# Kernel tuning notes

Measured on AMD Instinct MI355X. Metric: run time of the kernel, lower is better.

## Reference

```python
import jax, jax.numpy as jnp
import numpy as np

B, N, HID, E, H = 4, 256, 256, 64, 4
OUT = HID // 2          # 128
D = OUT // H            # 32
AGG = H * (2 * D + 1)   # 260 = concat(mean D, attn_sum 1, max D) per head


def setup_inputs() -> dict:
    key = jax.random.key(0)
    ks = jax.random.split(key, 7)
    s = 0.05
    return {
        "h_x": jax.random.normal(ks[0], (B, N, HID), jnp.float32),
        "h_e": jax.random.normal(ks[1], (B, N, N, E), jnp.float32),
        "h_m": jnp.ones((B, N), jnp.float32),
        "W_Q": jax.random.normal(ks[2], (OUT, HID), jnp.float32) * s,
        "W_K": jax.random.normal(ks[3], (OUT, E), jnp.float32) * s,
        "W_V": jax.random.normal(ks[4], (OUT, E), jnp.float32) * s,
        "W_R": jax.random.normal(ks[5], (OUT, AGG), jnp.float32) * s,
    }


def reference(h_x, h_e, h_m, W_Q, W_K, W_V, W_R):
    # queries from node features: [B,H,N,D]
    h_q = (h_x @ W_Q.T).reshape(B, N, H, D).transpose(0, 2, 1, 3)
    # keys/values from dense pairwise edge features: [B,H,N,N,D]
    h_k = jnp.einsum('bnme,ce->bnmc', h_e, W_K).reshape(B, N, N, H, D).transpose(0, 3, 1, 2, 4)
    h_v = jnp.einsum('bnme,ce->bnmc', h_e, W_V).reshape(B, N, N, H, D).transpose(0, 3, 1, 2, 4)
    # broadcast dot: [B,H,N,N]
    scores = jnp.einsum('bhnd,bhnmd->bhnm', h_q, h_k) / np.float32(np.sqrt(D))
    # per-node mask broadcast as [B,1,N,1] (masks query rows)
    scores = jnp.where(h_m[:, None, :, None] == 0, -jnp.inf, scores)
    # NOTE: original code softmaxes over dim=1 = HEAD axis (faithful)
    attn = jax.nn.softmax(scores, axis=1)                      # [B,H,N,N]
    attn_w = attn[..., None] * h_v                             # [B,H,N,N,D]
    aggr_sum = attn_w.sum(axis=3)                              # [B,H,N,D]
    attn_sum = attn.sum(axis=3, keepdims=True) + 1e-8          # [B,H,N,1]
    aggr_mean = aggr_sum / attn_sum
    aggr_max = attn_w.max(axis=3)                              # [B,H,N,D]
    multi = jnp.concatenate([aggr_mean, attn_sum, aggr_max], axis=-1)  # [B,H,N,2D+1]
    aggr_out = multi.transpose(0, 2, 1, 3).reshape(B, N, AGG)  # [B,N,260]
    return aggr_out @ W_R.T                                    # [B,N,OUT]
```

## Files before the change

kernel.cpp:

```cpp
#include <hip/hip_runtime.h>

constexpr int Bb   = 4;
constexpr int Nn   = 256;
constexpr int HID  = 256;
constexpr int Ee   = 64;
constexpr int Hh   = 4;
constexpr int OUTc = 128;
constexpr int Dd   = 32;
constexpr int AGG  = 260;

constexpr int MT    = 32;
constexpr int A_LD  = 72;
constexpr int KV_LD = 260;

typedef __attribute__((ext_vector_type(8))) short short8;
typedef __attribute__((ext_vector_type(4))) float floatx4;

__device__ __forceinline__ unsigned short f2bf(float f) {
    union { float f; unsigned u; } x; x.f = f;
    unsigned r = x.u + 0x7FFFu + ((x.u >> 16) & 1u);
    return (unsigned short)(r >> 16);
}

__device__ __forceinline__ short8 pack8(floatx4 f0, floatx4 f1) {
    short8 v;
    v[0] = (short)f2bf(f0[0]); v[1] = (short)f2bf(f0[1]);
    v[2] = (short)f2bf(f0[2]); v[3] = (short)f2bf(f0[3]);
    v[4] = (short)f2bf(f1[0]); v[5] = (short)f2bf(f1[1]);
    v[6] = (short)f2bf(f1[2]); v[7] = (short)f2bf(f1[3]);
    return v;
}

__global__ __launch_bounds__(256, 3)
void eama_fused(const float* __restrict__ h_x, const float* __restrict__ h_e,
                const float* __restrict__ h_m, const float* __restrict__ W_Q,
                const float* __restrict__ W_K, const float* __restrict__ W_V,
                const float* __restrict__ W_R, float* __restrict__ out)
{
    __shared__ __align__(16) unsigned short sA[MT * A_LD];
    __shared__ __align__(16) float sKV[MT * KV_LD];
    __shared__ __align__(16) float sQ[OUTc];
    __shared__ float sSc[MT][4];
    __shared__ float sAt[MT][4];
    __shared__ float sAsum[Hh];
    __shared__ float sRed[2][OUTc];
    __shared__ __align__(16) float sMulti[AGG];

    const int tid  = threadIdx.x;
    const int lane = tid & 63;
    const int wv   = tid >> 6;
    const int bn   = blockIdx.x;
    const float maskv = h_m[bn];

    short8 bfrag[4][2];
    {
        const int ncol = lane & 15;
        const int q8   = lane >> 4;
        #pragma unroll
        for (int ct = 0; ct < 4; ++ct) {
            const int c = wv * 64 + ct * 16 + ncol;
            const float* row = (c < OUTc) ? (W_K + c * Ee) : (W_V + (c - OUTc) * Ee);
            #pragma unroll
            for (int ks = 0; ks < 2; ++ks) {
                const int k0 = ks * 32 + q8 * 8;
                floatx4 f0 = *(const floatx4*)(row + k0);
                floatx4 f1 = *(const floatx4*)(row + k0 + 4);
                bfrag[ct][ks] = pack8(f0, f1);
            }
        }
    }

    {
        float* sHx = sKV;
        sHx[tid] = h_x[bn * HID + tid];
        __syncthreads();
        if (tid < OUTc) {
            const float* wq = W_Q + tid * HID;
            float acc = 0.f;
            #pragma unroll 8
            for (int e = 0; e < HID; e += 4) {
                floatx4 w4 = *(const floatx4*)(wq + e);
                floatx4 x4 = *(const floatx4*)(sHx + e);
                acc += w4[0]*x4[0] + w4[1]*x4[1] + w4[2]*x4[2] + w4[3]*x4[3];
            }
            sQ[tid] = acc;
        }
        __syncthreads();
    }

    float vsum = 0.f, vmax = -3.402823466e38f;
    float asum_acc = 0.f;
    const int hf = tid >> 7;
    const int cp = tid & 127;
    const int hd = cp >> 5;

    const float* heb = h_e + (size_t)bn * (Nn * Ee);

    for (int tile = 0; tile < Nn / MT; ++tile) {
        const int m0 = tile * MT;
        __syncthreads();
        {
            const int r = tid >> 3, blk = tid & 7;
            const float* src = heb + (m0 + r) * Ee + blk * 8;
            floatx4 f0 = *(const floatx4*)(src);
            floatx4 f1 = *(const floatx4*)(src + 4);
            *(short8*)&sA[r * A_LD + blk * 8] = pack8(f0, f1);
        }
        __syncthreads();
        {
            const int ncol = lane & 15;
            const int q8   = lane >> 4;
            floatx4 acc[2][4];
            #pragma unroll
            for (int mt = 0; mt < 2; ++mt)
                #pragma unroll
                for (int ct = 0; ct < 4; ++ct)
                    acc[mt][ct] = (floatx4){0.f, 0.f, 0.f, 0.f};
            #pragma unroll
            for (int ks = 0; ks < 2; ++ks) {
                short8 a0 = *(const short8*)&sA[(ncol) * A_LD + ks * 32 + q8 * 8];
                short8 a1 = *(const short8*)&sA[(16 + ncol) * A_LD + ks * 32 + q8 * 8];
                #pragma unroll
                for (int ct = 0; ct < 4; ++ct) {
                    acc[0][ct] = __builtin_amdgcn_mfma_f32_16x16x32_bf16(a0, bfrag[ct][ks], acc[0][ct], 0, 0, 0);
                    acc[1][ct] = __builtin_amdgcn_mfma_f32_16x16x32_bf16(a1, bfrag[ct][ks], acc[1][ct], 0, 0, 0);
                }
            }
            #pragma unroll
            for (int mt = 0; mt < 2; ++mt) {
                const int rowb = mt * 16 + q8 * 4;
                #pragma unroll
                for (int ct = 0; ct < 4; ++ct) {
                    const int col = wv * 64 + ct * 16 + ncol;
                    #pragma unroll
                    for (int r = 0; r < 4; ++r)
                        sKV[(rowb + r) * KV_LD + col] = acc[mt][ct][r];
                }
            }
        }
        __syncthreads();
        if (tid < 128) {
            const int m = tid & 31, h = tid >> 5;
            const float* kvr = &sKV[m * KV_LD + h * Dd];
            const float* qr  = &sQ[h * Dd];
            float p = 0.f;
            #pragma unroll
            for (int d = 0; d < Dd; d += 4) {
                floatx4 k4 = *(const floatx4*)(kvr + d);
                floatx4 q4 = *(const floatx4*)(qr + d);
                p += k4[0]*q4[0] + k4[1]*q4[1] + k4[2]*q4[2] + k4[3]*q4[3];
            }
            p *= 0.1767766952966369f;
            sSc[m][h] = (maskv != 0.f) ? p : -1e30f;
        }
        __syncthreads();
        if (tid < MT) {
            float s0 = sSc[tid][0], s1 = sSc[tid][1], s2 = sSc[tid][2], s3 = sSc[tid][3];
            float mx = fmaxf(fmaxf(s0, s1), fmaxf(s2, s3));
            float e0 = __expf(s0 - mx), e1 = __expf(s1 - mx);
            float e2 = __expf(s2 - mx), e3 = __expf(s3 - mx);
            float inv = 1.f / (e0 + e1 + e2 + e3);
            sAt[tid][0] = e0 * inv; sAt[tid][1] = e1 * inv;
            sAt[tid][2] = e2 * inv; sAt[tid][3] = e3 * inv;
        }
        __syncthreads();
        #pragma unroll
        for (int mm = 0; mm < MT / 2; ++mm) {
            const int m = hf * (MT / 2) + mm;
            const float a  = sAt[m][hd];
            const float vv = sKV[m * KV_LD + OUTc + cp];
            const float aw = a * vv;
            vsum += aw;
            vmax = fmaxf(vmax, aw);
        }
        if (tid < Hh) {
            #pragma unroll
            for (int m = 0; m < MT; ++m) asum_acc += sAt[m][tid];
        }
    }

    __syncthreads();
    if (hf) { sRed[0][cp] = vsum; sRed[1][cp] = vmax; }
    if (tid < Hh) sAsum[tid] = asum_acc + 1e-8f;
    __syncthreads();
    if (tid < OUTc) {
        const float vs = vsum + sRed[0][tid];
        const float vm = fmaxf(vmax, sRed[1][tid]);
        const int h = tid >> 5, d = tid & 31;
        sMulti[h * 65 + d]      = vs / sAsum[h];
        sMulti[h * 65 + 33 + d] = vm;
        if (tid < Hh) sMulti[tid * 65 + 32] = sAsum[tid];
    }
    __syncthreads();
    if (tid < OUTc) {
        const float* wr = W_R + tid * AGG;
        float acc = 0.f;
        #pragma unroll 5
        for (int j = 0; j < AGG; j += 4) {
            floatx4 w4 = *(const floatx4*)(wr + j);
            floatx4 m4 = *(const floatx4*)(&sMulti[j]);
            acc += w4[0]*m4[0] + w4[1]*m4[1] + w4[2]*m4[2] + w4[3]*m4[3];
        }
        out[bn * OUTc + tid] = acc;
    }
}

extern "C" void kernel_launch(void* const* d_in, const int* in_sizes, int n_in,
                              void* d_out, int out_size, void* d_ws, size_t ws_size,
                              hipStream_t stream) {
    const float* h_x = (const float*)d_in[0];
    const float* h_e = (const float*)d_in[1];
    const float* h_m = (const float*)d_in[2];
    const float* W_Q = (const float*)d_in[3];
    const float* W_K = (const float*)d_in[4];
    const float* W_V = (const float*)d_in[5];
    const float* W_R = (const float*)d_in[6];
    float* out = (float*)d_out;
    eama_fused<<<dim3(Bb * Nn), dim3(256), 0, stream>>>(h_x, h_e, h_m, W_Q, W_K, W_V, W_R, out);
}
```

Measured before the change: 151.0 us.

## Split fused kernel into Q projection, split-N partial stage, and reduction stage

Moves the Q projection into a separate batched kernel and splits the per-node loop over neighbor tiles across a second grid dimension, so each block handles only 64 neighbors and writes partial sum/max/attention-sum records to workspace. A third kernel reduces the partials and applies W_R. Inside stage1, the V half is consumed straight from MFMA accumulators with shuffle reductions instead of being staged through shared memory, and h_e loads are prefetched into registers. This is meant to raise parallelism and occupancy and shrink LDS use, at the cost of two extra launches and a workspace round trip.

```diff
diff --git a/kernel.cpp b/kernel.cpp
--- a/kernel.cpp
+++ b/kernel.cpp
@@ -10,8 +10,11 @@
 constexpr int AGG  = 260;
 
 constexpr int MT    = 32;
+constexpr int TPB   = 2;
+constexpr int NTP   = Nn / (MT * TPB);
 constexpr int A_LD  = 72;
-constexpr int KV_LD = 260;
+constexpr int K_LD  = 132;
+constexpr int REC   = 264;
 
 typedef __attribute__((ext_vector_type(8))) short short8;
 typedef __attribute__((ext_vector_type(4))) float floatx4;
@@ -31,101 +34,102 @@
     return v;
 }
 
-__global__ __launch_bounds__(256, 3)
-void eama_fused(const float* __restrict__ h_x, const float* __restrict__ h_e,
-                const float* __restrict__ h_m, const float* __restrict__ W_Q,
-                const float* __restrict__ W_K, const float* __restrict__ W_V,
-                const float* __restrict__ W_R, float* __restrict__ out)
+__global__ __launch_bounds__(256)
+void eama_q(const float* __restrict__ h_x, const float* __restrict__ W_Q,
+            float* __restrict__ qbuf)
+{
+    __shared__ __align__(16) float sHx[16 * HID];
+    const int t = threadIdx.x;
+    const int b0 = blockIdx.x * 16;
+    for (int i = t; i < 16 * HID; i += 256)
+        sHx[i] = h_x[b0 * HID + i];
+    __syncthreads();
+    const int c = t & 127, rh = t >> 7;
+    const float* wq = W_Q + c * HID;
+    for (int rr = rh; rr < 16; rr += 2) {
+        const float* xr = &sHx[rr * HID];
+        float acc = 0.f;
+        #pragma unroll 8
+        for (int e = 0; e < HID; e += 4) {
+            floatx4 w4 = *(const floatx4*)(wq + e);
+            floatx4 x4 = *(const floatx4*)(xr + e);
+            acc += w4[0]*x4[0] + w4[1]*x4[1] + w4[2]*x4[2] + w4[3]*x4[3];
+        }
+        qbuf[(b0 + rr) * OUTc + c] = acc;
+    }
+}
+
+__global__ __launch_bounds__(256, 4)
+void eama_stage1(const float* __restrict__ h_e, const float* __restrict__ h_m,
+                 const float* __restrict__ W_K, const float* __restrict__ W_V,
+                 const float* __restrict__ qbuf, float* __restrict__ wsP)
 {
     __shared__ __align__(16) unsigned short sA[MT * A_LD];
-    __shared__ __align__(16) float sKV[MT * KV_LD];
+    __shared__ __align__(16) float sK[MT * K_LD];
     __shared__ __align__(16) float sQ[OUTc];
     __shared__ float sSc[MT][4];
     __shared__ float sAt[MT][4];
-    __shared__ float sAsum[Hh];
-    __shared__ float sRed[2][OUTc];
-    __shared__ __align__(16) float sMulti[AGG];
 
     const int tid  = threadIdx.x;
     const int lane = tid & 63;
     const int wv   = tid >> 6;
+    const int ncol = lane & 15;
+    const int q8   = lane >> 4;
     const int bn   = blockIdx.x;
+    const int tp   = blockIdx.y;
     const float maskv = h_m[bn];
 
+    if (tid < OUTc) sQ[tid] = qbuf[bn * OUTc + tid];
+
+    const float* heb = h_e + ((size_t)bn * Nn + tp * (MT * TPB)) * Ee;
+    const int r = tid >> 3, blk = tid & 7;
+    floatx4 pf[TPB][2];
+    #pragma unroll
+    for (int it = 0; it < TPB; ++it) {
+        const float* src = heb + (it * MT + r) * Ee + blk * 8;
+        pf[it][0] = *(const floatx4*)(src);
+        pf[it][1] = *(const floatx4*)(src + 4);
+    }
+
     short8 bfrag[4][2];
-    {
-        const int ncol = lane & 15;
-        const int q8   = lane >> 4;
-        #pragma unroll
-        for (int ct = 0; ct < 4; ++ct) {
-            const int c = wv * 64 + ct * 16 + ncol;
-            const float* row = (c < OUTc) ? (W_K + c * Ee) : (W_V + (c - OUTc) * Ee);
-            #pragma unroll
-            for (int ks = 0; ks < 2; ++ks) {
-                const int k0 = ks * 32 + q8 * 8;
-                floatx4 f0 = *(const floatx4*)(row + k0);
-                floatx4 f1 = *(const floatx4*)(row + k0 + 4);
-                bfrag[ct][ks] = pack8(f0, f1);
-            }
-        }
-    }
-
-    {
-        float* sHx = sKV;
-        sHx[tid] = h_x[bn * HID + tid];
-        __syncthreads();
-        if (tid < OUTc) {
-            const float* wq = W_Q + tid * HID;
-            float acc = 0.f;
-            #pragma unroll 8
-            for (int e = 0; e < HID; e += 4) {
-                floatx4 w4 = *(const floatx4*)(wq + e);
-                floatx4 x4 = *(const floatx4*)(sHx + e);
-                acc += w4[0]*x4[0] + w4[1]*x4[1] + w4[2]*x4[2] + w4[3]*x4[3];
-            }
-            sQ[tid] = acc;
-        }
-        __syncthreads();
-    }
-
-    float vsum = 0.f, vmax = -3.402823466e38f;
-    float asum_acc = 0.f;
-    const int hf = tid >> 7;
-    const int cp = tid & 127;
-    const int hd = cp >> 5;
-
-    const float* heb = h_e + (size_t)bn * (Nn * Ee);
-
-    for (int tile = 0; tile < Nn / MT; ++tile) {
-        const int m0 = tile * MT;
-        __syncthreads();
-        {
-            const int r = tid >> 3, blk = tid & 7;
-            const float* src = heb + (m0 + r) * Ee + blk * 8;
-            floatx4 f0 = *(const floatx4*)(src);
-            floatx4 f1 = *(const floatx4*)(src + 4);
-            *(short8*)&sA[r * A_LD + blk * 8] = pack8(f0, f1);
-        }
-        __syncthreads();
-        {
-            const int ncol = lane & 15;
-            const int q8   = lane >> 4;
-            floatx4 acc[2][4];
-            #pragma unroll
-            for (int mt = 0; mt < 2; ++mt)
-                #pragma unroll
-                for (int ct = 0; ct < 4; ++ct)
-                    acc[mt][ct] = (floatx4){0.f, 0.f, 0.f, 0.f};
-            #pragma unroll
-            for (int ks = 0; ks < 2; ++ks) {
-                short8 a0 = *(const short8*)&sA[(ncol) * A_LD + ks * 32 + q8 * 8];
-                short8 a1 = *(const short8*)&sA[(16 + ncol) * A_LD + ks * 32 + q8 * 8];
-                #pragma unroll
-                for (int ct = 0; ct < 4; ++ct) {
-                    acc[0][ct] = __builtin_amdgcn_mfma_f32_16x16x32_bf16(a0, bfrag[ct][ks], acc[0][ct], 0, 0, 0);
-                    acc[1][ct] = __builtin_amdgcn_mfma_f32_16x16x32_bf16(a1, bfrag[ct][ks], acc[1][ct], 0, 0, 0);
-                }
-            }
+    #pragma unroll
+    for (int ct = 0; ct < 4; ++ct) {
+        const int c = wv * 64 + ct * 16 + ncol;
+        const float* row = (c < OUTc) ? (W_K + c * Ee) : (W_V + (c - OUTc) * Ee);
+        #pragma unroll
+        for (int ks = 0; ks < 2; ++ks) {
+            const int k0 = ks * 32 + q8 * 8;
+            floatx4 f0 = *(const floatx4*)(row + k0);
+            floatx4 f1 = *(const floatx4*)(row + k0 + 4);
+            bfrag[ct][ks] = pack8(f0, f1);
+        }
+    }
+
+    float vs[4], vm[4], asum = 0.f;
+    #pragma unroll
+    for (int ct = 0; ct < 4; ++ct) { vs[ct] = 0.f; vm[ct] = -3.402823466e38f; }
+
+    for (int it = 0; it < TPB; ++it) {
+        *(short8*)&sA[r * A_LD + blk * 8] = pack8(pf[it][0], pf[it][1]);
+        __syncthreads();
+
+        floatx4 acc[2][4];
+        #pragma unroll
+        for (int mt = 0; mt < 2; ++mt)
+            #pragma unroll
+            for (int ct = 0; ct < 4; ++ct)
+                acc[mt][ct] = (floatx4){0.f, 0.f, 0.f, 0.f};
+        #pragma unroll
+        for (int ks = 0; ks < 2; ++ks) {
+            short8 a0 = *(const short8*)&sA[(ncol) * A_LD + ks * 32 + q8 * 8];
+            short8 a1 = *(const short8*)&sA[(16 + ncol) * A_LD + ks * 32 + q8 * 8];
+            #pragma unroll
+            for (int ct = 0; ct < 4; ++ct) {
+                acc[0][ct] = __builtin_amdgcn_mfma_f32_16x16x32_bf16(a0, bfrag[ct][ks], acc[0][ct], 0, 0, 0);
+                acc[1][ct] = __builtin_amdgcn_mfma_f32_16x16x32_bf16(a1, bfrag[ct][ks], acc[1][ct], 0, 0, 0);
+            }
+        }
+        if (wv < 2) {
             #pragma unroll
             for (int mt = 0; mt < 2; ++mt) {
                 const int rowb = mt * 16 + q8 * 4;
@@ -133,20 +137,21 @@
                 for (int ct = 0; ct < 4; ++ct) {
                     const int col = wv * 64 + ct * 16 + ncol;
                     #pragma unroll
-                    for (int r = 0; r < 4; ++r)
-                        sKV[(rowb + r) * KV_LD + col] = acc[mt][ct][r];
+                    for (int rr = 0; rr < 4; ++rr)
+                        sK[(rowb + rr) * K_LD + col] = acc[mt][ct][rr];
                 }
             }
         }
         __syncthreads();
+
         if (tid < 128) {
             const int m = tid & 31, h = tid >> 5;
-            const float* kvr = &sKV[m * KV_LD + h * Dd];
-            const float* qr  = &sQ[h * Dd];
+            const float* kr = &sK[m * K_LD + h * Dd];
+            const float* qr = &sQ[h * Dd];
             float p = 0.f;
             #pragma unroll
             for (int d = 0; d < Dd; d += 4) {
-                floatx4 k4 = *(const floatx4*)(kvr + d);
+                floatx4 k4 = *(const floatx4*)(kr + d);
                 floatx4 q4 = *(const floatx4*)(qr + d);
                 p += k4[0]*q4[0] + k4[1]*q4[1] + k4[2]*q4[2] + k4[3]*q4[3];
             }
@@ -154,6 +159,7 @@
             sSc[m][h] = (maskv != 0.f) ? p : -1e30f;
         }
         __syncthreads();
+
         if (tid < MT) {
             float s0 = sSc[tid][0], s1 = sSc[tid][1], s2 = sSc[tid][2], s3 = sSc[tid][3];
             float mx = fmaxf(fmaxf(s0, s1), fmaxf(s2, s3));
@@ -164,41 +170,87 @@
             sAt[tid][2] = e2 * inv; sAt[tid][3] = e3 * inv;
         }
         __syncthreads();
-        #pragma unroll
-        for (int mm = 0; mm < MT / 2; ++mm) {
-            const int m = hf * (MT / 2) + mm;
-            const float a  = sAt[m][hd];
-            const float vv = sKV[m * KV_LD + OUTc + cp];
-            const float aw = a * vv;
-            vsum += aw;
-            vmax = fmaxf(vmax, aw);
+
+        if (wv >= 2) {
+            #pragma unroll
+            for (int ct = 0; ct < 4; ++ct) {
+                const int hd = (wv - 2) * 2 + (ct >> 1);
+                #pragma unroll
+                for (int mt = 0; mt < 2; ++mt) {
+                    const int rowb = mt * 16 + q8 * 4;
+                    #pragma unroll
+                    for (int rr = 0; rr < 4; ++rr) {
+                        const float aw = sAt[rowb + rr][hd] * acc[mt][ct][rr];
+                        vs[ct] += aw;
+                        vm[ct] = fmaxf(vm[ct], aw);
+                    }
+                }
+            }
         }
         if (tid < Hh) {
             #pragma unroll
-            for (int m = 0; m < MT; ++m) asum_acc += sAt[m][tid];
-        }
-    }
-
+            for (int m = 0; m < MT; ++m) asum += sAt[m][tid];
+        }
+    }
+
+    const size_t base = ((size_t)bn * NTP + tp) * REC;
+    if (wv >= 2) {
+        #pragma unroll
+        for (int ct = 0; ct < 4; ++ct) {
+            vs[ct] += __shfl_xor(vs[ct], 16, 64);
+            vs[ct] += __shfl_xor(vs[ct], 32, 64);
+            vm[ct] = fmaxf(vm[ct], __shfl_xor(vm[ct], 16, 64));
+            vm[ct] = fmaxf(vm[ct], __shfl_xor(vm[ct], 32, 64));
+        }
+        if (lane < 16) {
+            #pragma unroll
+            for (int ct = 0; ct < 4; ++ct) {
+                const int cv = (wv - 2) * 64 + ct * 16 + ncol;
+                wsP[base + cv]        = vs[ct];
+                wsP[base + OUTc + cv] = vm[ct];
+            }
+        }
+    }
+    if (tid < Hh) wsP[base + 2 * OUTc + tid] = asum;
+}
+
+__global__ __launch_bounds__(128)
+void eama_stage2(const float* __restrict__ wsP, const float* __restrict__ W_R,
+                 float* __restrict__ out)
+{
+    __shared__ __align__(16) float sM[REC];
+    __shared__ float sAs[Hh];
+    const int tid = threadIdx.x;
+    const int bn  = blockIdx.x;
+    const size_t base = (size_t)bn * NTP * REC;
+
+    float vsum = 0.f, vmax = -3.402823466e38f;
+    #pragma unroll
+    for (int tp = 0; tp < NTP; ++tp) {
+        vsum += wsP[base + tp * REC + tid];
+        vmax = fmaxf(vmax, wsP[base + tp * REC + OUTc + tid]);
+    }
+    if (tid < Hh) {
+        float a = 1e-8f;
+        #pragma unroll
+        for (int tp = 0; tp < NTP; ++tp) a += wsP[base + tp * REC + 2 * OUTc + tid];
+        sAs[tid] = a;
+    }
     __syncthreads();
-    if (hf) { sRed[0][cp] = vsum; sRed[1][cp] = vmax; }
-    if (tid < Hh) sAsum[tid] = asum_acc + 1e-8f;
+    {
+        const int h = tid >> 5, d = tid & 31;
+        sM[h * 65 + d]      = vsum / sAs[h];
+        sM[h * 65 + 33 + d] = vmax;
+        if (tid < Hh) sM[tid * 65 + 32] = sAs[tid];
+    }
     __syncthreads();
-    if (tid < OUTc) {
-        const float vs = vsum + sRed[0][tid];
-        const float vm = fmaxf(vmax, sRed[1][tid]);
-        const int h = tid >> 5, d = tid & 31;
-        sMulti[h * 65 + d]      = vs / sAsum[h];
-        sMulti[h * 65 + 33 + d] = vm;
-        if (tid < Hh) sMulti[tid * 65 + 32] = sAsum[tid];
-    }
-    __syncthreads();
-    if (tid < OUTc) {
+    {
         const float* wr = W_R + tid * AGG;
         float acc = 0.f;
         #pragma unroll 5
         for (int j = 0; j < AGG; j += 4) {
             floatx4 w4 = *(const floatx4*)(wr + j);
-            floatx4 m4 = *(const floatx4*)(&sMulti[j]);
+            floatx4 m4 = *(const floatx4*)(&sM[j]);
             acc += w4[0]*m4[0] + w4[1]*m4[1] + w4[2]*m4[2] + w4[3]*m4[3];
         }
         out[bn * OUTc + tid] = acc;
@@ -215,6 +267,11 @@
     const float* W_K = (const float*)d_in[4];
     const float* W_V = (const float*)d_in[5];
     const float* W_R = (const float*)d_in[6];
-    float* out = (float*)d_out;
-    eama_fused<<<dim3(Bb * Nn), dim3(256), 0, stream>>>(h_x, h_e, h_m, W_Q, W_K, W_V, W_R, out);
-}
+    float* out  = (float*)d_out;
+    float* wsP  = (float*)d_ws;
+    float* qbuf = wsP + (size_t)Bb * Nn * NTP * REC;
+
+    eama_q<<<dim3(Bb * Nn / 16), dim3(256), 0, stream>>>(h_x, W_Q, qbuf);
+    eama_stage1<<<dim3(Bb * Nn, NTP), dim3(256), 0, stream>>>(h_e, h_m, W_K, W_V, qbuf, wsP);
+    eama_stage2<<<dim3(Bb * Nn), dim3(128), 0, stream>>>(wsP, W_R, out);
+}
```

New measurement: 198.1 us. +31.1%, slower.
